# Performance work log

Measured on AMD Instinct MI355X. Metric: run time of the kernel, lower is better.

## Reference

```python
import jax, jax.numpy as jnp
import numpy as np

B = 2048       # batch
N = 256        # num_memory_locations
M = 64         # memory_size
U = 512        # num_units
IN = 10        # num_bits_per_vector + 2
SHIFT = 1      # conv_shift_range
CLIP = 20.0


def setup_inputs() -> dict:
    key = jax.random.key(0)
    ks = jax.random.split(key, 20)
    s = 0.05
    A0 = jax.random.uniform(ks[5], (2, B, N), dtype=jnp.float32)
    A0 = A0 / jnp.sum(A0, axis=-1, keepdims=True)  # distribution-like prev attention
    return {
        'x_t':  jax.random.normal(ks[0], (B, IN), dtype=jnp.float32),
        'H0':   jax.random.normal(ks[1], (B, U), dtype=jnp.float32) * s,
        'C0':   jax.random.normal(ks[2], (B, U), dtype=jnp.float32) * s,
        'm0':   jax.random.normal(ks[3], (B, N, M), dtype=jnp.float32) * s,
        'R0':   jax.random.normal(ks[4], (B, M), dtype=jnp.float32) * s,
        'A0':   A0,
        'Wprep': jax.random.normal(ks[6], (M, U), dtype=jnp.float32) * s,
        'bprep': jnp.zeros((U,), dtype=jnp.float32),
        'Wx':   jax.random.normal(ks[7], (IN + U, 4 * U), dtype=jnp.float32) * s,
        'Wh':   jax.random.normal(ks[8], (U, 4 * U), dtype=jnp.float32) * s,
        'bl':   jnp.zeros((4 * U,), dtype=jnp.float32),
        'Wr':   jax.random.normal(ks[9], (U, M + 6), dtype=jnp.float32) * s,
        'br':   jnp.zeros((M + 6,), dtype=jnp.float32),
        'Ww':   jax.random.normal(ks[10], (U, 3 * M + 6), dtype=jnp.float32) * s,
        'bw':   jnp.zeros((3 * M + 6,), dtype=jnp.float32),
        'Wo':   jax.random.normal(ks[11], (U + M, U), dtype=jnp.float32) * s,
        'bo':   jnp.zeros((U,), dtype=jnp.float32),
    }


def _addressing(head, m_tm1, a_tm1):
    # head: (B, >=M+6); m_tm1: (B,N,M); a_tm1: (B,N)
    k = jnp.tanh(head[:, :M])                                   # (B,M)
    beta = jax.nn.softplus(head[:, M])                          # (B,)
    g = jax.nn.sigmoid(head[:, M + 1])                          # (B,)
    s = jax.nn.softmax(head[:, M + 2:M + 2 + 2 * SHIFT + 1], axis=-1)  # (B,3)
    gamma = jax.nn.softplus(head[:, M + 2 + 2 * SHIFT + 1])     # (B,)
    # cosine similarity content addressing
    ip = jnp.einsum('bnm,bm->bn', m_tm1, k)                     # (B,N)
    k_norm = jnp.sqrt(jnp.sum(k * k, axis=1, keepdims=True))    # (B,1)
    m_norm = jnp.sqrt(jnp.sum(m_tm1 * m_tm1, axis=2))           # (B,N)
    K = ip / (k_norm * m_norm + 1e-8)
    w_c = jax.nn.softmax(beta[:, None] * K, axis=1)             # exp/sum == softmax
    w_g = g[:, None] * w_c + (1.0 - g[:, None]) * a_tm1
    # circular convolution: s placed at offsets [0..SHIFT] and [-SHIFT..-1]
    s_full = jnp.concatenate(
        [s[:, :SHIFT + 1], jnp.zeros((s.shape[0], N - (2 * SHIFT + 1)), s.dtype), s[:, -SHIFT:]],
        axis=1)                                                 # (B,N)
    idx = (jnp.arange(N)[:, None] - jnp.arange(N)[None, :]) % N  # (N,N)
    w_conv = jnp.einsum('bij,bj->bi', s_full[:, idx], w_g)       # w[i]=sum_j w_g[j]*s[(i-j)%N]
    w_sharp = w_conv ** gamma[:, None]
    return w_sharp / jnp.sum(w_sharp, axis=1, keepdims=True)


def reference(x_t, H0, C0, m0, R0, A0, Wprep, bprep, Wx, Wh, bl, Wr, br, Ww, bw, Wo, bo):
    # prep from previous reads
    h = R0 @ Wprep + bprep                                      # (B,U)
    # single-layer LSTM controller
    z = jnp.concatenate([x_t, h], axis=1) @ Wx + H0 @ Wh + bl   # (B,4U)
    i, f, g_, o = jnp.split(z, 4, axis=1)
    c_t = jax.nn.sigmoid(f) * C0 + jax.nn.sigmoid(i) * jnp.tanh(g_)
    h = jax.nn.sigmoid(o) * jnp.tanh(c_t)
    h = jnp.clip(h, -CLIP, CLIP)
    # heads
    r_out = h @ Wr + br                                         # (B, M+6)
    w_out = h @ Ww + bw                                         # (B, 3M+6)
    w_read = _addressing(r_out, m0, A0[0])                      # (B,N)
    w_write = _addressing(w_out, m0, A0[1])                     # (B,N)
    # read from OLD memory (as in original)
    R_t = jnp.einsum('bn,bnm->bm', w_read, m0)                  # (B,M)
    # write: erase + add
    del_v = jax.nn.sigmoid(w_out[:, -2 * M:-M])                 # (B,M)
    add_v = jnp.tanh(w_out[:, -M:])                             # (B,M)
    ww = w_write[:, :, None]                                    # (B,N,1)
    m_t = m0 * (1.0 - ww * del_v[:, None, :]) + ww * add_v[:, None, :]
    y_t = jnp.clip(jnp.concatenate([h, R_t], axis=1) @ Wo + bo, -CLIP, CLIP)
    return (y_t, m_t, R_t, w_read, w_write)
```

## Files before the change

### kernel.cpp

```cpp
#include <hip/hip_runtime.h>


using u16   = unsigned short;
using bfrag = __attribute__((ext_vector_type(8))) short;
using f4    = __attribute__((ext_vector_type(4))) float;

__device__ __forceinline__ float bf2f(u16 s){ union{float f;unsigned u;}v; v.u=((unsigned)s)<<16; return v.f; }
__device__ __forceinline__ u16 f2bf(float f){ union{float f;unsigned u;}v; v.f=f; unsigned r=v.u+0x7fffu+((v.u>>16)&1u); return (u16)(r>>16); }
__device__ __forceinline__ void bfpair(unsigned pr, float&a, float&b){ union{float f;unsigned u;}x,y; x.u=pr<<16; y.u=pr&0xffff0000u; a=x.f; b=y.f; }
__device__ __forceinline__ unsigned packbf(float a, float b){ return (unsigned)f2bf(a) | ((unsigned)f2bf(b)<<16); }
__device__ __forceinline__ float sigm(float x){ return 1.f/(1.f+expf(-x)); }
__device__ __forceinline__ float softplus_(float x){ return fmaxf(x,0.f)+log1pf(expf(-fabsf(x))); }

__device__ __forceinline__ void gld16(const u16* g, u16* l){
    __builtin_amdgcn_global_load_lds((const __attribute__((address_space(1))) unsigned*)g,
                                     (__attribute__((address_space(3))) unsigned*)l, 16, 0, 0);
}


__global__ __launch_bounds__(256) void k_wt_lstm(const float* __restrict__ Wx, const float* __restrict__ Wh,
                                                 u16* __restrict__ Wt){
    __shared__ float t[32][33];
    int n0 = blockIdx.x*32, k0 = blockIdx.y*32;
    int tx = threadIdx.x & 31, ty = threadIdx.x >> 5;
    #pragma unroll
    for(int r=0;r<4;r++){
        int k = k0 + ty*4 + r, n = n0 + tx;
        float v;
        if(k < 522)       v = Wx[k*2048 + n];
        else if(k < 1034) v = Wh[(k-522)*2048 + n];
        else              v = 0.f;
        t[ty*4+r][tx] = v;
    }
    __syncthreads();
    #pragma unroll
    for(int r=0;r<4;r++){
        int n = n0 + ty*4 + r, k = k0 + tx;
        Wt[n*1056 + k] = f2bf(t[tx][ty*4+r]);
    }
}

__global__ __launch_bounds__(256) void k_wt_heads(const float* __restrict__ Wr, const float* __restrict__ Ww,
                                                  u16* __restrict__ Wt){
    __shared__ float t[32][33];
    int n0 = blockIdx.x*32, k0 = blockIdx.y*32;
    int tx = threadIdx.x & 31, ty = threadIdx.x >> 5;
    #pragma unroll
    for(int r=0;r<4;r++){
        int k = k0 + ty*4 + r, n = n0 + tx;
        float v;
        if(n < 70)        v = Wr[k*70 + n];
        else if(n < 268)  v = Ww[k*198 + (n-70)];
        else              v = 0.f;
        t[ty*4+r][tx] = v;
    }
    __syncthreads();
    #pragma unroll
    for(int r=0;r<4;r++){
        int n = n0 + ty*4 + r, k = k0 + tx;
        Wt[n*512 + k] = f2bf(t[tx][ty*4+r]);
    }
}

__global__ __launch_bounds__(256) void k_wt_out(const float* __restrict__ Wo, u16* __restrict__ Wt){
    __shared__ float t[32][33];
    int n0 = blockIdx.x*32, k0 = blockIdx.y*32;
    int tx = threadIdx.x & 31, ty = threadIdx.x >> 5;
    #pragma unroll
    for(int r=0;r<4;r++){
        int k = k0 + ty*4 + r, n = n0 + tx;
        t[ty*4+r][tx] = Wo[k*512 + n];
    }
    __syncthreads();
    #pragma unroll
    for(int r=0;r<4;r++){
        int n = n0 + ty*4 + r, k = k0 + tx;
        Wt[n*576 + k] = f2bf(t[tx][ty*4+r]);
    }
}

__global__ __launch_bounds__(256) void k_abuild(const float* __restrict__ x, const float* __restrict__ H0,
                                                const float* __restrict__ R0, const float* __restrict__ Wprep,
                                                const float* __restrict__ bprep, u16* __restrict__ A){
    int flat = blockIdx.x*256 + threadIdx.x;
    int b = flat >> 9, u = flat & 511;
    u16* Ab = A + (size_t)b*1056;
    float acc = bprep[u];
    const float* r = R0 + b*64;
    #pragma unroll 8
    for(int m=0;m<64;m++) acc += r[m] * Wprep[m*512+u];
    Ab[10+u] = f2bf(acc);
    Ab[522+u] = f2bf(H0[b*512+u]);
    if(u<10) Ab[u] = f2bf(x[b*10+u]);
    if(u<22) Ab[1034+u] = 0;
}

__device__ __forceinline__ void gemm128(const u16* __restrict__ A, int lda,
                                        const u16* __restrict__ Bt, int ldb,
                                        int bm, int bn, int kiters,
                                        u16* Al, u16* Bl, f4 acc[4][4]){
    int tid = threadIdx.x, w = tid>>6, lane = tid&63, quad = lane>>4, l16 = lane&15;
    int wr = w>>1, wc = w&1;
    f4 z4 = {0.f,0.f,0.f,0.f};
    #pragma unroll
    for(int i=0;i<4;i++)
        #pragma unroll
        for(int j=0;j<4;j++) acc[i][j] = z4;
    int rA0 = tid>>2, kc = tid&3;
    int rA1 = rA0 + 64;
    const u16* ga0 = A  + (size_t)(bm+rA0)*lda + kc*8;
    const u16* ga1 = A  + (size_t)(bm+rA1)*lda + kc*8;
    const u16* gb0 = Bt + (size_t)(bn+rA0)*ldb + kc*8;
    const u16* gb1 = Bt + (size_t)(bn+rA1)*ldb + kc*8;
    u16* lA0 = Al + (w*64)*8;
    u16* lA1 = Al + (256 + w*64)*8;
    u16* lB0 = Bl + (w*64)*8;
    u16* lB1 = Bl + (256 + w*64)*8;
    for(int kt=0; kt<kiters; kt++){
        __syncthreads();
        gld16(ga0, lA0); gld16(ga1, lA1);
        gld16(gb0, lB0); gld16(gb1, lB1);
        ga0 += 32; ga1 += 32; gb0 += 32; gb1 += 32;
        __syncthreads();
        bfrag af[4], bf[4];
        #pragma unroll
        for(int i=0;i<4;i++) af[i] = *(const bfrag*)&Al[(wr*64 + i*16 + l16)*32 + quad*8];
        #pragma unroll
        for(int j=0;j<4;j++) bf[j] = *(const bfrag*)&Bl[(wc*64 + j*16 + l16)*32 + quad*8];
        #pragma unroll
        for(int i=0;i<4;i++)
            #pragma unroll
            for(int j=0;j<4;j++)
                acc[i][j] = __builtin_amdgcn_mfma_f32_16x16x32_bf16(af[i], bf[j], acc[i][j], 0, 0, 0);
    }
}

__global__ __launch_bounds__(256) void k_gemm_lstm(const u16* __restrict__ A, const u16* __restrict__ Wt,
                                                   float* __restrict__ z){
    __shared__ u16 Al[128*32], Bl[128*32];
    f4 acc[4][4];
    int bm = blockIdx.x*128, bn = blockIdx.y*128;
    gemm128(A, 1056, Wt, 1056, bm, bn, 33, Al, Bl, acc);
    int lane = threadIdx.x&63, quad = lane>>4, l16 = lane&15, w = threadIdx.x>>6;
    int wr = w>>1, wc = w&1;
    #pragma unroll
    for(int i=0;i<4;i++){
        #pragma unroll
        for(int j=0;j<4;j++){
            int col = bn + wc*64 + j*16 + l16;
            #pragma unroll
            for(int r=0;r<4;r++){
                int row = bm + wr*64 + i*16 + quad*4 + r;
                z[(size_t)row*2048 + col] = acc[i][j][r];
            }
        }
    }
}

__global__ __launch_bounds__(256) void k_gates(const float* __restrict__ z, const float* __restrict__ C0,
                                               const float* __restrict__ bl, u16* __restrict__ A2){
    int flat = blockIdx.x*256 + threadIdx.x;
    int b = flat>>9, u = flat&511;
    const float* zb = z + (size_t)b*2048;
    float zi = zb[u]      + bl[u];
    float zf = zb[512+u]  + bl[512+u];
    float zg = zb[1024+u] + bl[1024+u];
    float zo = zb[1536+u] + bl[1536+u];
    float c  = sigm(zf)*C0[b*512+u] + sigm(zi)*tanhf(zg);
    float hv = sigm(zo)*tanhf(c);
    hv = fminf(fmaxf(hv,-20.f),20.f);
    A2[(size_t)b*576 + u] = f2bf(hv);
}

__global__ __launch_bounds__(256) void k_gemm_heads(const u16* __restrict__ A2, const u16* __restrict__ Wt,
                                                    const float* __restrict__ br, const float* __restrict__ bw,
                                                    float* __restrict__ rout, float* __restrict__ wout){
    __shared__ u16 Al[128*32], Bl[128*32];
    f4 acc[4][4];
    int bm = blockIdx.x*128, bn = blockIdx.y*128;
    gemm128(A2, 576, Wt, 512, bm, bn, 16, Al, Bl, acc);
    int lane = threadIdx.x&63, quad = lane>>4, l16 = lane&15, w = threadIdx.x>>6;
    int wr = w>>1, wc = w&1;
    #pragma unroll
    for(int i=0;i<4;i++){
        #pragma unroll
        for(int j=0;j<4;j++){
            int col = bn + wc*64 + j*16 + l16;
            if(col >= 268) continue;
            #pragma unroll
            for(int r=0;r<4;r++){
                int row = bm + wr*64 + i*16 + quad*4 + r;
                float v = acc[i][j][r];
                if(col < 70) rout[(size_t)row*70 + col]        = v + br[col];
                else         wout[(size_t)row*198 + (col-70)]  = v + bw[col-70];
            }
        }
    }
}

__global__ __launch_bounds__(256) void k_gemm_out(const u16* __restrict__ A2, const u16* __restrict__ Wt,
                                                  const float* __restrict__ bo, float* __restrict__ y){
    __shared__ u16 Al[128*32], Bl[128*32];
    f4 acc[4][4];
    int bm = blockIdx.x*128, bn = blockIdx.y*128;
    gemm128(A2, 576, Wt, 576, bm, bn, 18, Al, Bl, acc);
    int lane = threadIdx.x&63, quad = lane>>4, l16 = lane&15, w = threadIdx.x>>6;
    int wr = w>>1, wc = w&1;
    #pragma unroll
    for(int i=0;i<4;i++){
        #pragma unroll
        for(int j=0;j<4;j++){
            int col = bn + wc*64 + j*16 + l16;
            float bias = bo[col];
            #pragma unroll
            for(int r=0;r<4;r++){
                int row = bm + wr*64 + i*16 + quad*4 + r;
                float v = acc[i][j][r] + bias;
                v = fminf(fmaxf(v,-20.f),20.f);
                y[(size_t)row*512 + col] = v;
            }
        }
    }
}

__device__ __forceinline__ float blk_sum(float* red, int tid, float v){
    red[tid]=v; __syncthreads();
    for(int s=128;s>0;s>>=1){ if(tid<s) red[tid]+=red[tid+s]; __syncthreads(); }
    float r=red[0]; __syncthreads(); return r;
}
__device__ __forceinline__ float blk_max(float* red, int tid, float v){
    red[tid]=v; __syncthreads();
    for(int s=128;s>0;s>>=1){ if(tid<s) red[tid]=fmaxf(red[tid],red[tid+s]); __syncthreads(); }
    float r=red[0]; __syncthreads(); return r;
}

__global__ __launch_bounds__(256) void k_addr(const float* __restrict__ m0, const float* __restrict__ A0,
                                              const float* __restrict__ rout, const float* __restrict__ wout,
                                              u16* __restrict__ A2,
                                              float* __restrict__ out_mt, float* __restrict__ out_rt,
                                              float* __restrict__ out_wr, float* __restrict__ out_ww){
    __shared__ u16   m0h[256*66];
    __shared__ float red[256];
    __shared__ float kk_s[64];
    __shared__ float wg_s[256];
    __shared__ float wsel[2][256];
    __shared__ float mnorm[256];
    __shared__ float sc[6];
    __shared__ float dv[64], avv[64];
    int tid = threadIdx.x; int b = blockIdx.x;

    const float* mb = m0 + (size_t)b*16384;
    #pragma unroll
    for(int i=0;i<16;i++){
        int e = i*1024 + tid*4;
        float4 v = *(const float4*)(mb + e);
        int n = e>>6, mcol = e&63;
        unsigned* dst = (unsigned*)&m0h[n*66 + mcol];
        dst[0] = packbf(v.x, v.y);
        dst[1] = packbf(v.z, v.w);
    }
    __syncthreads();
    {
        float s=0.f; const u16* row=&m0h[tid*66];
        #pragma unroll 8
        for(int m=0;m<64;m+=2){ float v0,v1; bfpair(*(const unsigned*)&row[m],v0,v1); s+=v0*v0+v1*v1; }
        mnorm[tid]=sqrtf(s);
    }
    __syncthreads();

    for(int head=0; head<2; head++){
        const float* hd = head ? (wout + b*198) : (rout + b*70);
        if(tid<64) kk_s[tid] = tanhf(hd[tid]);
        if(tid==64){
            sc[0]=softplus_(hd[64]);
            sc[1]=sigm(hd[65]);
            float e0=hd[66],e1=hd[67],e2=hd[68];
            float mx=fmaxf(e0,fmaxf(e1,e2));
            float x0=expf(e0-mx),x1=expf(e1-mx),x2=expf(e2-mx);
            float ss=x0+x1+x2;
            sc[2]=x0/ss; sc[3]=x1/ss; sc[4]=x2/ss;
            sc[5]=softplus_(hd[69]);
        }
        __syncthreads();
        float kv=(tid<64)?kk_s[tid]:0.f;
        float knorm = sqrtf(blk_sum(red,tid,kv*kv));
        float ip=0.f; const u16* row=&m0h[tid*66];
        #pragma unroll 8
        for(int m=0;m<64;m+=2){ float v0,v1; bfpair(*(const unsigned*)&row[m],v0,v1); ip += v0*kk_s[m]+v1*kk_s[m+1]; }
        float K = ip/(knorm*mnorm[tid] + 1e-8f);
        float e = sc[0]*K;
        float mx = blk_max(red,tid,e);
        float p = expf(e-mx);
        float wc = p / blk_sum(red,tid,p);
        float a = A0[head*524288 + b*256 + tid];
        float g = sc[1];
        float wg = g*wc + (1.f-g)*a;
        wg_s[tid]=wg; __syncthreads();
        float conv = sc[2]*wg + sc[3]*wg_s[(tid+255)&255] + sc[4]*wg_s[(tid+1)&255];
        conv = fmaxf(conv, 1e-35f);
        float wsh = expf(sc[5]*logf(conv));
        float w = wsh / blk_sum(red,tid,wsh);
        wsel[head][tid]=w;
        (head ? out_ww : out_wr)[b*256 + tid] = w;
        __syncthreads();
    }
    {
        int chunk=tid>>6, m=tid&63;
        float p=0.f;
        #pragma unroll 8
        for(int j=0;j<64;j++){ int n=chunk*64+j; p += wsel[0][n]*bf2f(m0h[n*66+m]); }
        red[tid]=p; __syncthreads();
        if(tid<64){
            float rt = red[tid]+red[tid+64]+red[tid+128]+red[tid+192];
            out_rt[b*64+tid]=rt;
            A2[(size_t)b*576 + 512 + tid] = f2bf(rt);
        }
        __syncthreads();
    }
    {
        const float* wob = wout + b*198;
        if(tid<64){ dv[tid]=sigm(wob[70+tid]); avv[tid]=tanhf(wob[134+tid]); }
        __syncthreads();
        #pragma unroll
        for(int i=0;i<16;i++){
            int e = i*1024 + tid*4; int n=e>>6; int mcol=e&63;
            float ww = wsel[1][n];
            const unsigned* src = (const unsigned*)&m0h[n*66+mcol];
            float v0,v1,v2,v3;
            bfpair(src[0],v0,v1);
            bfpair(src[1],v2,v3);
            float4 o;
            o.x = v0*(1.f-ww*dv[mcol])   + ww*avv[mcol];
            o.y = v1*(1.f-ww*dv[mcol+1]) + ww*avv[mcol+1];
            o.z = v2*(1.f-ww*dv[mcol+2]) + ww*avv[mcol+2];
            o.w = v3*(1.f-ww*dv[mcol+3]) + ww*avv[mcol+3];
            *(float4*)(out_mt + (size_t)b*16384 + e) = o;
        }
    }
}

extern "C" void kernel_launch(void* const* d_in, const int* in_sizes, int n_in,
                              void* d_out, int out_size, void* d_ws, size_t ws_size,
                              hipStream_t stream) {
    const float* x     = (const float*)d_in[0];
    const float* H0    = (const float*)d_in[1];
    const float* C0    = (const float*)d_in[2];
    const float* m0    = (const float*)d_in[3];
    const float* R0    = (const float*)d_in[4];
    const float* A0    = (const float*)d_in[5];
    const float* Wprep = (const float*)d_in[6];
    const float* bprep = (const float*)d_in[7];
    const float* Wx    = (const float*)d_in[8];
    const float* Wh    = (const float*)d_in[9];
    const float* bl    = (const float*)d_in[10];
    const float* Wr    = (const float*)d_in[11];
    const float* br    = (const float*)d_in[12];
    const float* Ww    = (const float*)d_in[13];
    const float* bw    = (const float*)d_in[14];
    const float* Wo    = (const float*)d_in[15];
    const float* bo    = (const float*)d_in[16];

    float* ws = (float*)d_ws;
    u16*   Wt_lstm = (u16*)(ws + 0);
    u16*   Wt_h    = (u16*)(ws + 1081344);
    u16*   Wt_o    = (u16*)(ws + 1179648);
    u16*   Abuf    = (u16*)(ws + 1327104);
    u16*   A2      = (u16*)(ws + 2408448);
    float* z       =        ws + 2998272;
    float* rout    =        ws + 7192576;
    float* wout    =        ws + 7335936;

    float* out    = (float*)d_out;
    float* out_y  = out;
    float* out_mt = out + 1048576;
    float* out_rt = out + 34603008;
    float* out_wr = out + 34734080;
    float* out_ww = out + 35258368;

    hipLaunchKernelGGL(k_wt_lstm,  dim3(64,33), dim3(256), 0, stream, Wx, Wh, Wt_lstm);
    hipLaunchKernelGGL(k_wt_heads, dim3(12,16), dim3(256), 0, stream, Wr, Ww, Wt_h);
    hipLaunchKernelGGL(k_wt_out,   dim3(16,18), dim3(256), 0, stream, Wo, Wt_o);
    hipLaunchKernelGGL(k_abuild,   dim3(4096),  dim3(256), 0, stream, x, H0, R0, Wprep, bprep, Abuf);
    hipLaunchKernelGGL(k_gemm_lstm, dim3(16,16), dim3(256), 0, stream, Abuf, Wt_lstm, z);
    hipLaunchKernelGGL(k_gates,    dim3(4096),  dim3(256), 0, stream, z, C0, bl, A2);
    hipLaunchKernelGGL(k_gemm_heads, dim3(16,3), dim3(256), 0, stream, A2, Wt_h, br, bw, rout, wout);
    hipLaunchKernelGGL(k_addr,     dim3(2048),  dim3(256), 0, stream, m0, A0, rout, wout, A2,
                       out_mt, out_rt, out_wr, out_ww);
    hipLaunchKernelGGL(k_gemm_out, dim3(16,4),  dim3(256), 0, stream, A2, Wt_o, bo, out_y);
}
```

Baseline: 397.3 us.

## Restructure addressing kernel: wave-shuffle reductions, fused heads, fused read with memory write

The addressing kernel now processes both heads together, with one pass over the memory rows computing the norm and both inner products. Tree reductions that needed many barriers are replaced by 64-lane shuffle reductions plus a small cross-wave combine. The read vector is accumulated inside the erase/add write loop, which removes a separate pass over LDS. Head scalars, erase/add vectors and A0 loads are set up in parallel before the first barrier, which cuts the barrier count and redundant LDS traffic at the cost of somewhat higher register pressure.

```diff
diff --git a/kernel.cpp b/kernel.cpp
--- a/kernel.cpp
+++ b/kernel.cpp
@@ -223,118 +223,171 @@
     }
 }
 
-__device__ __forceinline__ float blk_sum(float* red, int tid, float v){
-    red[tid]=v; __syncthreads();
-    for(int s=128;s>0;s>>=1){ if(tid<s) red[tid]+=red[tid+s]; __syncthreads(); }
-    float r=red[0]; __syncthreads(); return r;
-}
-__device__ __forceinline__ float blk_max(float* red, int tid, float v){
-    red[tid]=v; __syncthreads();
-    for(int s=128;s>0;s>>=1){ if(tid<s) red[tid]=fmaxf(red[tid],red[tid+s]); __syncthreads(); }
-    float r=red[0]; __syncthreads(); return r;
-}
-
 __global__ __launch_bounds__(256) void k_addr(const float* __restrict__ m0, const float* __restrict__ A0,
                                               const float* __restrict__ rout, const float* __restrict__ wout,
                                               u16* __restrict__ A2,
                                               float* __restrict__ out_mt, float* __restrict__ out_rt,
                                               float* __restrict__ out_wr, float* __restrict__ out_ww){
     __shared__ u16   m0h[256*66];
-    __shared__ float red[256];
-    __shared__ float kk_s[64];
-    __shared__ float wg_s[256];
+    __shared__ float kk_s[2][64];
+    __shared__ float knorm_s[2];
+    __shared__ float sc[2][6];
+    __shared__ float wgrr[512];
     __shared__ float wsel[2][256];
-    __shared__ float mnorm[256];
-    __shared__ float sc[6];
     __shared__ float dv[64], avv[64];
-    int tid = threadIdx.x; int b = blockIdx.x;
+    __shared__ float wpart[4][6];
+    int tid = threadIdx.x, b = blockIdx.x;
+    int lane = tid & 63, w = tid >> 6;
+
+    float a0r = A0[b*256 + tid];
+    float a1r = A0[524288 + b*256 + tid];
 
     const float* mb = m0 + (size_t)b*16384;
     #pragma unroll
     for(int i=0;i<16;i++){
         int e = i*1024 + tid*4;
         float4 v = *(const float4*)(mb + e);
-        int n = e>>6, mcol = e&63;
-        unsigned* dst = (unsigned*)&m0h[n*66 + mcol];
+        int n = e>>6, mc = e&63;
+        unsigned* dst = (unsigned*)&m0h[n*66 + mc];
         dst[0] = packbf(v.x, v.y);
         dst[1] = packbf(v.z, v.w);
     }
-    __syncthreads();
+
+    if(tid < 128){
+        int hh = tid >> 6, m = lane;
+        float kv = tanhf(hh ? wout[b*198 + m] : rout[b*70 + m]);
+        kk_s[hh][m] = kv;
+        float s2 = kv*kv;
+        #pragma unroll
+        for(int o=32;o>0;o>>=1) s2 += __shfl_xor(s2, o, 64);
+        if(m == 0) knorm_s[hh] = sqrtf(s2);
+    } else if(tid < 192){
+        int hh = tid - 128;
+        if(hh < 2){
+            const float* hd = hh ? (wout + b*198) : (rout + b*70);
+            sc[hh][0] = softplus_(hd[64]);
+            sc[hh][1] = sigm(hd[65]);
+            float e0=hd[66], e1=hd[67], e2=hd[68];
+            float mx = fmaxf(e0, fmaxf(e1, e2));
+            float x0=expf(e0-mx), x1=expf(e1-mx), x2=expf(e2-mx);
+            float ssum = x0+x1+x2;
+            sc[hh][2]=x0/ssum; sc[hh][3]=x1/ssum; sc[hh][4]=x2/ssum;
+            sc[hh][5] = softplus_(hd[69]);
+        }
+    } else {
+        int m = tid - 192;
+        dv[m]  = sigm(wout[b*198 + 70 + m]);
+        avv[m] = tanhf(wout[b*198 + 134 + m]);
+    }
+    __syncthreads();
+
+    float ip0=0.f, ip1=0.f, ssq=0.f;
     {
-        float s=0.f; const u16* row=&m0h[tid*66];
-        #pragma unroll 8
-        for(int m=0;m<64;m+=2){ float v0,v1; bfpair(*(const unsigned*)&row[m],v0,v1); s+=v0*v0+v1*v1; }
-        mnorm[tid]=sqrtf(s);
-    }
-    __syncthreads();
-
-    for(int head=0; head<2; head++){
-        const float* hd = head ? (wout + b*198) : (rout + b*70);
-        if(tid<64) kk_s[tid] = tanhf(hd[tid]);
-        if(tid==64){
-            sc[0]=softplus_(hd[64]);
-            sc[1]=sigm(hd[65]);
-            float e0=hd[66],e1=hd[67],e2=hd[68];
-            float mx=fmaxf(e0,fmaxf(e1,e2));
-            float x0=expf(e0-mx),x1=expf(e1-mx),x2=expf(e2-mx);
-            float ss=x0+x1+x2;
-            sc[2]=x0/ss; sc[3]=x1/ss; sc[4]=x2/ss;
-            sc[5]=softplus_(hd[69]);
+        const u16* row = &m0h[tid*66];
+        const float2* k0p = (const float2*)kk_s[0];
+        const float2* k1p = (const float2*)kk_s[1];
+        #pragma unroll
+        for(int m=0;m<64;m+=2){
+            float v0,v1; bfpair(*(const unsigned*)&row[m], v0, v1);
+            float2 ka = k0p[m>>1], kb = k1p[m>>1];
+            ssq += v0*v0 + v1*v1;
+            ip0 += v0*ka.x + v1*ka.y;
+            ip1 += v0*kb.x + v1*kb.y;
+        }
+    }
+    float mn = sqrtf(ssq);
+    float K0 = ip0 / (knorm_s[0]*mn + 1e-8f);
+    float K1 = ip1 / (knorm_s[1]*mn + 1e-8f);
+    float e0 = sc[0][0]*K0, e1 = sc[1][0]*K1;
+
+    float mx0 = e0, mx1 = e1;
+    #pragma unroll
+    for(int o=32;o>0;o>>=1){ mx0 = fmaxf(mx0, __shfl_xor(mx0,o,64)); mx1 = fmaxf(mx1, __shfl_xor(mx1,o,64)); }
+    if(lane == 0){ wpart[w][0] = mx0; wpart[w][1] = mx1; }
+    __syncthreads();
+    mx0 = fmaxf(fmaxf(wpart[0][0],wpart[1][0]), fmaxf(wpart[2][0],wpart[3][0]));
+    mx1 = fmaxf(fmaxf(wpart[0][1],wpart[1][1]), fmaxf(wpart[2][1],wpart[3][1]));
+    float p0 = expf(e0-mx0), p1 = expf(e1-mx1);
+    float s0 = p0, s1 = p1;
+    #pragma unroll
+    for(int o=32;o>0;o>>=1){ s0 += __shfl_xor(s0,o,64); s1 += __shfl_xor(s1,o,64); }
+    if(lane == 0){ wpart[w][2] = s0; wpart[w][3] = s1; }
+    __syncthreads();
+    s0 = wpart[0][2]+wpart[1][2]+wpart[2][2]+wpart[3][2];
+    s1 = wpart[0][3]+wpart[1][3]+wpart[2][3]+wpart[3][3];
+    float wc0 = p0/s0, wc1 = p1/s1;
+
+    float g0 = sc[0][1], g1 = sc[1][1];
+    float wg0 = g0*wc0 + (1.f-g0)*a0r;
+    float wg1 = g1*wc1 + (1.f-g1)*a1r;
+    wgrr[tid] = wg0; wgrr[256+tid] = wg1;
+    __syncthreads();
+    int nm1 = (tid+255)&255, np1 = (tid+1)&255;
+    float conv0 = sc[0][2]*wg0 + sc[0][3]*wgrr[nm1]     + sc[0][4]*wgrr[np1];
+    float conv1 = sc[1][2]*wg1 + sc[1][3]*wgrr[256+nm1] + sc[1][4]*wgrr[256+np1];
+    conv0 = fmaxf(conv0, 1e-35f);  conv1 = fmaxf(conv1, 1e-35f);
+    float wsh0 = expf(sc[0][5]*logf(conv0));
+    float wsh1 = expf(sc[1][5]*logf(conv1));
+    float t0 = wsh0, t1 = wsh1;
+    #pragma unroll
+    for(int o=32;o>0;o>>=1){ t0 += __shfl_xor(t0,o,64); t1 += __shfl_xor(t1,o,64); }
+    if(lane == 0){ wpart[w][4] = t0; wpart[w][5] = t1; }
+    __syncthreads();
+    t0 = wpart[0][4]+wpart[1][4]+wpart[2][4]+wpart[3][4];
+    t1 = wpart[0][5]+wpart[1][5]+wpart[2][5]+wpart[3][5];
+    float w0 = wsh0/t0, w1 = wsh1/t1;
+    wsel[0][tid] = w0; wsel[1][tid] = w1;
+    out_wr[b*256 + tid] = w0;
+    out_ww[b*256 + tid] = w1;
+    __syncthreads();
+
+    float r0=0.f, r1=0.f, r2=0.f, r3=0.f;
+    {
+        int mc = (tid&15)*4;
+        float d0=dv[mc], d1=dv[mc+1], d2=dv[mc+2], d3=dv[mc+3];
+        float A0v=avv[mc], A1v=avv[mc+1], A2v=avv[mc+2], A3v=avv[mc+3];
+        float* outb = out_mt + (size_t)b*16384;
+        #pragma unroll
+        for(int i=0;i<16;i++){
+            int e = i*1024 + tid*4;
+            int n = i*16 + (tid>>4);
+            float wwv = wsel[1][n], wrv = wsel[0][n];
+            const unsigned* src = (const unsigned*)&m0h[n*66 + mc];
+            float v0,v1,v2,v3;
+            bfpair(src[0], v0, v1);
+            bfpair(src[1], v2, v3);
+            float4 o;
+            o.x = v0*(1.f - wwv*d0) + wwv*A0v;
+            o.y = v1*(1.f - wwv*d1) + wwv*A1v;
+            o.z = v2*(1.f - wwv*d2) + wwv*A2v;
+            o.w = v3*(1.f - wwv*d3) + wwv*A3v;
+            *(float4*)(outb + e) = o;
+            r0 += wrv*v0; r1 += wrv*v1; r2 += wrv*v2; r3 += wrv*v3;
+        }
+    }
+    {
+        float* rred = wgrr;
+        int g = tid>>4, mc = (tid&15)*4;
+        if(g >= 8){
+            rred[(g-8)*64 + mc]   = r0;
+            rred[(g-8)*64 + mc+1] = r1;
+            rred[(g-8)*64 + mc+2] = r2;
+            rred[(g-8)*64 + mc+3] = r3;
         }
         __syncthreads();
-        float kv=(tid<64)?kk_s[tid]:0.f;
-        float knorm = sqrtf(blk_sum(red,tid,kv*kv));
-        float ip=0.f; const u16* row=&m0h[tid*66];
-        #pragma unroll 8
-        for(int m=0;m<64;m+=2){ float v0,v1; bfpair(*(const unsigned*)&row[m],v0,v1); ip += v0*kk_s[m]+v1*kk_s[m+1]; }
-        float K = ip/(knorm*mnorm[tid] + 1e-8f);
-        float e = sc[0]*K;
-        float mx = blk_max(red,tid,e);
-        float p = expf(e-mx);
-        float wc = p / blk_sum(red,tid,p);
-        float a = A0[head*524288 + b*256 + tid];
-        float g = sc[1];
-        float wg = g*wc + (1.f-g)*a;
-        wg_s[tid]=wg; __syncthreads();
-        float conv = sc[2]*wg + sc[3]*wg_s[(tid+255)&255] + sc[4]*wg_s[(tid+1)&255];
-        conv = fmaxf(conv, 1e-35f);
-        float wsh = expf(sc[5]*logf(conv));
-        float w = wsh / blk_sum(red,tid,wsh);
-        wsel[head][tid]=w;
-        (head ? out_ww : out_wr)[b*256 + tid] = w;
+        if(g < 8){
+            rred[g*64 + mc]   += r0;
+            rred[g*64 + mc+1] += r1;
+            rred[g*64 + mc+2] += r2;
+            rred[g*64 + mc+3] += r3;
+        }
         __syncthreads();
-    }
-    {
-        int chunk=tid>>6, m=tid&63;
-        float p=0.f;
-        #pragma unroll 8
-        for(int j=0;j<64;j++){ int n=chunk*64+j; p += wsel[0][n]*bf2f(m0h[n*66+m]); }
-        red[tid]=p; __syncthreads();
-        if(tid<64){
-            float rt = red[tid]+red[tid+64]+red[tid+128]+red[tid+192];
-            out_rt[b*64+tid]=rt;
+        if(tid < 64){
+            float rt = 0.f;
+            #pragma unroll
+            for(int g2=0; g2<8; g2++) rt += rred[g2*64 + tid];
+            out_rt[b*64 + tid] = rt;
             A2[(size_t)b*576 + 512 + tid] = f2bf(rt);
-        }
-        __syncthreads();
-    }
-    {
-        const float* wob = wout + b*198;
-        if(tid<64){ dv[tid]=sigm(wob[70+tid]); avv[tid]=tanhf(wob[134+tid]); }
-        __syncthreads();
-        #pragma unroll
-        for(int i=0;i<16;i++){
-            int e = i*1024 + tid*4; int n=e>>6; int mcol=e&63;
-            float ww = wsel[1][n];
-            const unsigned* src = (const unsigned*)&m0h[n*66+mcol];
-            float v0,v1,v2,v3;
-            bfpair(src[0],v0,v1);
-            bfpair(src[1],v2,v3);
-            float4 o;
-            o.x = v0*(1.f-ww*dv[mcol])   + ww*avv[mcol];
-            o.y = v1*(1.f-ww*dv[mcol+1]) + ww*avv[mcol+1];
-            o.z = v2*(1.f-ww*dv[mcol+2]) + ww*avv[mcol+2];
-            o.w = v3*(1.f-ww*dv[mcol+3]) + ww*avv[mcol+3];
-            *(float4*)(out_mt + (size_t)b*16384 + e) = o;
         }
     }
 }
```

After: 387.6 us. -2.4%, faster.
